# Performance work log

Measured on AMD Instinct MI355X. Metric: run time of the kernel, lower is better.

## Reference

```python
import jax, jax.numpy as jnp
import numpy as np

EPS = 1e-8  # torch cosine_similarity default eps


def setup_inputs() -> dict:
    key = jax.random.key(0)
    k1, k2, k3 = jax.random.split(key, 3)
    bsz, sent_len, cont_dim, mp_dim = 16, 512, 768, 20
    repres = jax.random.normal(k1, (bsz, sent_len, cont_dim), dtype=jnp.float32)
    max_att = jax.random.normal(k2, (bsz, sent_len, cont_dim), dtype=jnp.float32)
    # nn.Parameter initialized uniform_(-1, 1)
    weight = jax.random.uniform(k3, (mp_dim, cont_dim), dtype=jnp.float32, minval=-1.0, maxval=1.0)
    return {"repres": repres, "max_att": max_att, "weight": weight}


def reference(repres, max_att, weight):
    # Original math: a = repres[:,None,:] * w[None], b = max_att[:,None,:] * w[None]
    # cos = <a,b> / (max(||a||,eps) * max(||b||,eps)) along last dim.
    # Fused form: never materialize [N, mp_dim, cont_dim]; contract with w^2 directly.
    bsz, sent_len, cont_dim = repres.shape
    r = repres.reshape(-1, cont_dim)   # [N, D]
    m = max_att.reshape(-1, cont_dim)  # [N, D]
    w2 = weight * weight               # [P, D]
    dot = jnp.einsum('nd,pd->np', r * m, w2)              # [N, P]
    n1 = jnp.sqrt(jnp.einsum('nd,pd->np', r * r, w2))     # [N, P]
    n2 = jnp.sqrt(jnp.einsum('nd,pd->np', m * m, w2))     # [N, P]
    cos = dot / (jnp.maximum(n1, EPS) * jnp.maximum(n2, EPS))
    return cos.reshape(bsz, sent_len, weight.shape[0])
```

## Files before the change

### kernel.cpp

```cpp
#include <hip/hip_runtime.h>
#include <math.h>
#include <stdint.h>

static constexpr int D_DIM   = 768;
static constexpr int NP      = 20;
static constexpr int NROWS   = 8192;
static constexpr int ROWS_PB = 16;
static constexpr int BLOCKS  = NROWS / ROWS_PB;
static constexpr int KW      = 192;
static constexpr int KSLICE  = 32;
static constexpr int NSLICES = KW / KSLICE;

typedef short  short8  __attribute__((ext_vector_type(8)));
typedef float  float4v __attribute__((ext_vector_type(4)));

static constexpr int A_WAVE = 8192;
static constexpr int A_BUF  = 4096;
static constexpr int A_MAT  = 2048;
static constexpr int B_OFF  = 32768;
static constexpr int B_CSTR = 776 * 2;
static constexpr int LDS_SZ = B_OFF + NP * B_CSTR;

__device__ __forceinline__ void async_copy16(const void* g, void* l) {
  __builtin_amdgcn_global_load_lds(
      (const __attribute__((address_space(1))) unsigned int*)(uintptr_t)g,
      (__attribute__((address_space(3))) unsigned int*)(uint32_t)(uintptr_t)l,
      16, 0, 0);
}

__device__ __forceinline__ unsigned short bf16_rne(float x) {
  unsigned u = __float_as_uint(x);
  u += 0x7FFFu + ((u >> 16) & 1u);
  return (unsigned short)(u >> 16);
}
__device__ __forceinline__ float bf16f(unsigned short h) {
  return __uint_as_float(((unsigned)h) << 16);
}

__global__ __launch_bounds__(256) void atte_cos_mfma(
    const float* __restrict__ repres,
    const float* __restrict__ max_att,
    const float* __restrict__ weight,
    float* __restrict__ out)
{
  const int tid  = threadIdx.x;
  const int wave = tid >> 6;
  const int lane = tid & 63;
  const int row0 = blockIdx.x * ROWS_PB;
  const int k0   = wave * KW;
  const int part = lane >> 4;
  const int mrow = lane & 15;

  __shared__ __align__(16) char smem[LDS_SZ];
  char* a_base = smem + wave * A_WAVE;

  auto stage = [&](int s, int b) {
#pragma unroll
    for (int j = 0; j < 2; ++j) {
      const int slot = j * 64 + lane;
      const int row  = slot >> 3;
      const int gp   = slot & 7;
      const int gl   = (gp - 2 * (row & 3)) & 7;
      const float* gr = repres  + (size_t)(row0 + row) * D_DIM + k0 + s * KSLICE + gl * 4;
      const float* gm = max_att + (size_t)(row0 + row) * D_DIM + k0 + s * KSLICE + gl * 4;
      char* la = a_base + b * A_BUF + slot * 16;
      async_copy16(gr, la);
      async_copy16(gm, la + A_MAT);
    }
  };

  stage(0, 0);
  stage(1, 1);

  for (int col = 0; col < NP; ++col) {
#pragma unroll
    for (int j = 0; j < 3; ++j) {
      const int k = j * 256 + tid;
      const float wv = weight[col * D_DIM + k];
      *(unsigned short*)(smem + B_OFF + col * B_CSTR + k * 2) = bf16_rne(wv * wv);
    }
  }

  __syncthreads();

  const int a_off = mrow * 128 + (((part + (mrow & 3)) & 3) * 32);
  const char* b0p = smem + B_OFF + (lane & 15) * B_CSTR + (k0 + part * 8) * 2;
  const int c1col = min(16 + (lane & 15), NP - 1);
  const char* b1p = smem + B_OFF + c1col * B_CSTR + (k0 + part * 8) * 2;

  float4v acc[6] = {};

#pragma unroll
  for (int s = 0; s < NSLICES; ++s) {
    __builtin_amdgcn_s_waitcnt(0x0F74);
    const char* ab = a_base + (s & 1) * A_BUF;

    float rv[8], mv[8];
    *(float4*)&rv[0] = *(const float4*)(ab + a_off);
    *(float4*)&rv[4] = *(const float4*)(ab + a_off + 16);
    *(float4*)&mv[0] = *(const float4*)(ab + A_MAT + a_off);
    *(float4*)&mv[4] = *(const float4*)(ab + A_MAT + a_off + 16);

    short8 a0h, a0l, a1h, a2h;
#pragma unroll
    for (int j = 0; j < 8; ++j) {
      const float pm = rv[j] * mv[j];
      const float pr = rv[j] * rv[j];
      const float pq = mv[j] * mv[j];
      const unsigned short h = bf16_rne(pm);
      a0h[j] = (short)h;
      a0l[j] = (short)bf16_rne(pm - bf16f(h));
      a1h[j] = (short)bf16_rne(pr);
      a2h[j] = (short)bf16_rne(pq);
    }

    const short8 b0 = *(const short8*)(b0p + s * 64);
    const short8 b1 = *(const short8*)(b1p + s * 64);

    acc[0] = __builtin_amdgcn_mfma_f32_16x16x32_bf16(a0h, b0, acc[0], 0, 0, 0);
    acc[0] = __builtin_amdgcn_mfma_f32_16x16x32_bf16(a0l, b0, acc[0], 0, 0, 0);
    acc[1] = __builtin_amdgcn_mfma_f32_16x16x32_bf16(a0h, b1, acc[1], 0, 0, 0);
    acc[1] = __builtin_amdgcn_mfma_f32_16x16x32_bf16(a0l, b1, acc[1], 0, 0, 0);
    acc[2] = __builtin_amdgcn_mfma_f32_16x16x32_bf16(a1h, b0, acc[2], 0, 0, 0);
    acc[3] = __builtin_amdgcn_mfma_f32_16x16x32_bf16(a1h, b1, acc[3], 0, 0, 0);
    acc[4] = __builtin_amdgcn_mfma_f32_16x16x32_bf16(a2h, b0, acc[4], 0, 0, 0);
    acc[5] = __builtin_amdgcn_mfma_f32_16x16x32_bf16(a2h, b1, acc[5], 0, 0, 0);

    if (s + 2 < NSLICES) {
      __builtin_amdgcn_s_waitcnt(0xC07F);
      stage(s + 2, s & 1);
    }
  }

  __syncthreads();
#pragma unroll
  for (int qc = 0; qc < 6; ++qc)
    *(float4v*)(smem + ((qc * 4 + wave) * 64 + lane) * 16) = acc[qc];
  __syncthreads();

  if (wave < 2) {
    const int ct = wave;
    float4v c0 = {}, c1 = {}, c2 = {};
#pragma unroll
    for (int wv = 0; wv < 4; ++wv) {
      c0 += *(const float4v*)(smem + (((0 * 2 + ct) * 4 + wv) * 64 + lane) * 16);
      c1 += *(const float4v*)(smem + (((1 * 2 + ct) * 4 + wv) * 64 + lane) * 16);
      c2 += *(const float4v*)(smem + (((2 * 2 + ct) * 4 + wv) * 64 + lane) * 16);
    }
    const int col = ct * 16 + (lane & 15);
    if (col < NP) {
      const int rbase = row0 + (lane >> 4) * 4;
#pragma unroll
      for (int r = 0; r < 4; ++r) {
        const float n1 = fmaxf(sqrtf(c1[r]), 1e-8f);
        const float n2 = fmaxf(sqrtf(c2[r]), 1e-8f);
        out[(size_t)(rbase + r) * NP + col] = c0[r] / (n1 * n2);
      }
    }
  }
}

extern "C" void kernel_launch(void* const* d_in, const int* in_sizes, int n_in,
                              void* d_out, int out_size, void* d_ws, size_t ws_size,
                              hipStream_t stream) {
  const float* repres  = (const float*)d_in[0];
  const float* max_att = (const float*)d_in[1];
  const float* weight  = (const float*)d_in[2];
  float* out = (float*)d_out;

  atte_cos_mfma<<<BLOCKS, 256, 0, stream>>>(repres, max_att, weight, out);
}
```

Baseline: 88.19 us.

## Replace bf16 MFMA kernel with fp32 FMA kernel staging full rows and squared weights

Replaces the split-bf16 MFMA kernel with an fp32 FMA kernel using 512 threads per block. Each block stages all 16 rows of both inputs in two halves via async global-to-LDS copies, and keeps the full fp32 squared weight table in about 156 KB of dynamic LDS. Each thread accumulates 60 dot products over a k-slice, and partial sums are combined with shuffles and then through LDS scratch. This drops the bf16 hi/lo emulation and the MFMA operand packing, and gains full fp32 accuracy. In exchange, the LDS footprint allows only one block per CU, each block re-reads and re-squares the full weight table, and there is little load/compute overlap.

```diff
diff --git a/kernel.cpp b/kernel.cpp
--- a/kernel.cpp
+++ b/kernel.cpp
@@ -1,25 +1,23 @@
 #include <hip/hip_runtime.h>
 #include <math.h>
 #include <stdint.h>
+
 
 static constexpr int D_DIM   = 768;
 static constexpr int NP      = 20;
 static constexpr int NROWS   = 8192;
 static constexpr int ROWS_PB = 16;
-static constexpr int BLOCKS  = NROWS / ROWS_PB;
-static constexpr int KW      = 192;
-static constexpr int KSLICE  = 32;
-static constexpr int NSLICES = KW / KSLICE;
+static constexpr int NBLK    = NROWS / ROWS_PB;
+static constexpr int NTHR    = 512;
 
-typedef short  short8  __attribute__((ext_vector_type(8)));
-typedef float  float4v __attribute__((ext_vector_type(4)));
+static constexpr int HALF_B  = 1536;
+static constexpr int MAT_B   = ROWS_PB * HALF_B;
+static constexpr int SWEEP_B = 2 * MAT_B;
+static constexpr int W2_OFF  = 2 * SWEEP_B;
+static constexpr int LDS_B   = W2_OFF + NP * D_DIM * 4;
 
-static constexpr int A_WAVE = 8192;
-static constexpr int A_BUF  = 4096;
-static constexpr int A_MAT  = 2048;
-static constexpr int B_OFF  = 32768;
-static constexpr int B_CSTR = 776 * 2;
-static constexpr int LDS_SZ = B_OFF + NP * B_CSTR;
+static constexpr int SCR_K   = 12;
+static constexpr int SCR_RND = 8 * NP * 3 * SCR_K;
 
 __device__ __forceinline__ void async_copy16(const void* g, void* l) {
   __builtin_amdgcn_global_load_lds(
@@ -28,145 +26,142 @@
       16, 0, 0);
 }
 
-__device__ __forceinline__ unsigned short bf16_rne(float x) {
-  unsigned u = __float_as_uint(x);
-  u += 0x7FFFu + ((u >> 16) & 1u);
-  return (unsigned short)(u >> 16);
-}
-__device__ __forceinline__ float bf16f(unsigned short h) {
-  return __uint_as_float(((unsigned)h) << 16);
-}
-
-__global__ __launch_bounds__(256) void atte_cos_mfma(
+__global__ __launch_bounds__(NTHR, 2) void atte_cos_v2(
     const float* __restrict__ repres,
     const float* __restrict__ max_att,
     const float* __restrict__ weight,
     float* __restrict__ out)
 {
+  extern __shared__ __align__(16) char smem[];
   const int tid  = threadIdx.x;
   const int wave = tid >> 6;
   const int lane = tid & 63;
   const int row0 = blockIdx.x * ROWS_PB;
-  const int k0   = wave * KW;
-  const int part = lane >> 4;
-  const int mrow = lane & 15;
 
-  __shared__ __align__(16) char smem[LDS_SZ];
-  char* a_base = smem + wave * A_WAVE;
-
-  auto stage = [&](int s, int b) {
+  auto dma_sweep = [&](int s) {
 #pragma unroll
-    for (int j = 0; j < 2; ++j) {
-      const int slot = j * 64 + lane;
-      const int row  = slot >> 3;
-      const int gp   = slot & 7;
-      const int gl   = (gp - 2 * (row & 3)) & 7;
-      const float* gr = repres  + (size_t)(row0 + row) * D_DIM + k0 + s * KSLICE + gl * 4;
-      const float* gm = max_att + (size_t)(row0 + row) * D_DIM + k0 + s * KSLICE + gl * 4;
-      char* la = a_base + b * A_BUF + slot * 16;
-      async_copy16(gr, la);
-      async_copy16(gm, la + A_MAT);
+    for (int i = 0; i < 6; ++i) {
+      const int ls  = wave * 6144 + i * 1024 + lane * 16;
+      const int mat = ls >= MAT_B;
+      const int off = ls - (mat ? MAT_B : 0);
+      const int r   = off / HALF_B;
+      const int kb  = off - r * HALF_B;
+      const char* src = (const char*)(mat ? max_att : repres)
+                      + (size_t)(row0 + r) * 3072 + (size_t)s * HALF_B + kb;
+      async_copy16(src, smem + s * SWEEP_B + ls);
     }
   };
 
-  stage(0, 0);
-  stage(1, 1);
+  dma_sweep(0);
 
-  for (int col = 0; col < NP; ++col) {
-#pragma unroll
-    for (int j = 0; j < 3; ++j) {
-      const int k = j * 256 + tid;
-      const float wv = weight[col * D_DIM + k];
-      *(unsigned short*)(smem + B_OFF + col * B_CSTR + k * 2) = bf16_rne(wv * wv);
+  {
+    const float4* wsrc = (const float4*)weight;
+    float4* wdst = (float4*)(smem + W2_OFF);
+    for (int idx = tid; idx < NP * D_DIM / 4; idx += NTHR) {
+      float4 w = wsrc[idx];
+      w.x *= w.x; w.y *= w.y; w.z *= w.z; w.w *= w.w;
+      wdst[idx] = w;
     }
   }
 
-  __syncthreads();
+  dma_sweep(1);
 
-  const int a_off = mrow * 128 + (((part + (mrow & 3)) & 3) * 32);
-  const char* b0p = smem + B_OFF + (lane & 15) * B_CSTR + (k0 + part * 8) * 2;
-  const int c1col = min(16 + (lane & 15), NP - 1);
-  const char* b1p = smem + B_OFF + c1col * B_CSTR + (k0 + part * 8) * 2;
+  const int row  = tid >> 5;
+  const int ksub = tid & 31;
 
-  float4v acc[6] = {};
+  float accd[NP], acc1[NP], acc2[NP];
+#pragma unroll
+  for (int p = 0; p < NP; ++p) { accd[p] = 0.f; acc1[p] = 0.f; acc2[p] = 0.f; }
+
+  auto compute_half = [&](const int s) {
+    const char* ar = smem + s * SWEEP_B + row * HALF_B;
+    const char* am = ar + MAT_B;
+    const char* wb = smem + W2_OFF + s * HALF_B;
+#pragma unroll
+    for (int j = 0; j < 3; ++j) {
+      const int g16 = (ksub + 32 * j) * 16;
+      const float4 r4 = *(const float4*)(ar + g16);
+      const float4 m4 = *(const float4*)(am + g16);
+      const float pd0 = r4.x * m4.x, pd1 = r4.y * m4.y, pd2 = r4.z * m4.z, pd3 = r4.w * m4.w;
+      const float p10 = r4.x * r4.x, p11 = r4.y * r4.y, p12 = r4.z * r4.z, p13 = r4.w * r4.w;
+      const float p20 = m4.x * m4.x, p21 = m4.y * m4.y, p22 = m4.z * m4.z, p23 = m4.w * m4.w;
+#pragma unroll
+      for (int p = 0; p < NP; ++p) {
+        const float4 w4 = *(const float4*)(wb + p * 3072 + g16);
+        accd[p] = fmaf(pd3, w4.w, fmaf(pd2, w4.z, fmaf(pd1, w4.y, fmaf(pd0, w4.x, accd[p]))));
+        acc1[p] = fmaf(p13, w4.w, fmaf(p12, w4.z, fmaf(p11, w4.y, fmaf(p10, w4.x, acc1[p]))));
+        acc2[p] = fmaf(p23, w4.w, fmaf(p22, w4.z, fmaf(p21, w4.y, fmaf(p20, w4.x, acc2[p]))));
+      }
+    }
+  };
+
+  __builtin_amdgcn_sched_barrier(0);
+  __builtin_amdgcn_s_waitcnt(0x0076);
+  __builtin_amdgcn_s_barrier();
+  __builtin_amdgcn_sched_barrier(0);
+  compute_half(0);
+
+  __builtin_amdgcn_sched_barrier(0);
+  __builtin_amdgcn_s_waitcnt(0x0F70);
+  __builtin_amdgcn_s_barrier();
+  __builtin_amdgcn_sched_barrier(0);
+  compute_half(1);
 
 #pragma unroll
-  for (int s = 0; s < NSLICES; ++s) {
-    __builtin_amdgcn_s_waitcnt(0x0F74);
-    const char* ab = a_base + (s & 1) * A_BUF;
+  for (int p = 0; p < NP; ++p) {
+    accd[p] += __shfl_xor(accd[p], 16); acc1[p] += __shfl_xor(acc1[p], 16); acc2[p] += __shfl_xor(acc2[p], 16);
+    accd[p] += __shfl_xor(accd[p],  8); acc1[p] += __shfl_xor(acc1[p],  8); acc2[p] += __shfl_xor(acc2[p],  8);
+  }
 
-    float rv[8], mv[8];
-    *(float4*)&rv[0] = *(const float4*)(ab + a_off);
-    *(float4*)&rv[4] = *(const float4*)(ab + a_off + 16);
-    *(float4*)&mv[0] = *(const float4*)(ab + A_MAT + a_off);
-    *(float4*)&mv[4] = *(const float4*)(ab + A_MAT + a_off + 16);
+  __builtin_amdgcn_sched_barrier(0);
+  __builtin_amdgcn_s_waitcnt(0xC07F);
+  __builtin_amdgcn_s_barrier();
+  __builtin_amdgcn_sched_barrier(0);
 
-    short8 a0h, a0l, a1h, a2h;
+  float* scr = (float*)smem;
+  if (ksub < 8) {
+    const int rnd = row >> 3, lrow = row & 7;
+    float* base = scr + rnd * SCR_RND + (lrow * NP * 3) * SCR_K + ksub;
 #pragma unroll
-    for (int j = 0; j < 8; ++j) {
-      const float pm = rv[j] * mv[j];
-      const float pr = rv[j] * rv[j];
-      const float pq = mv[j] * mv[j];
-      const unsigned short h = bf16_rne(pm);
-      a0h[j] = (short)h;
-      a0l[j] = (short)bf16_rne(pm - bf16f(h));
-      a1h[j] = (short)bf16_rne(pr);
-      a2h[j] = (short)bf16_rne(pq);
-    }
-
-    const short8 b0 = *(const short8*)(b0p + s * 64);
-    const short8 b1 = *(const short8*)(b1p + s * 64);
-
-    acc[0] = __builtin_amdgcn_mfma_f32_16x16x32_bf16(a0h, b0, acc[0], 0, 0, 0);
-    acc[0] = __builtin_amdgcn_mfma_f32_16x16x32_bf16(a0l, b0, acc[0], 0, 0, 0);
-    acc[1] = __builtin_amdgcn_mfma_f32_16x16x32_bf16(a0h, b1, acc[1], 0, 0, 0);
-    acc[1] = __builtin_amdgcn_mfma_f32_16x16x32_bf16(a0l, b1, acc[1], 0, 0, 0);
-    acc[2] = __builtin_amdgcn_mfma_f32_16x16x32_bf16(a1h, b0, acc[2], 0, 0, 0);
-    acc[3] = __builtin_amdgcn_mfma_f32_16x16x32_bf16(a1h, b1, acc[3], 0, 0, 0);
-    acc[4] = __builtin_amdgcn_mfma_f32_16x16x32_bf16(a2h, b0, acc[4], 0, 0, 0);
-    acc[5] = __builtin_amdgcn_mfma_f32_16x16x32_bf16(a2h, b1, acc[5], 0, 0, 0);
-
-    if (s + 2 < NSLICES) {
-      __builtin_amdgcn_s_waitcnt(0xC07F);
-      stage(s + 2, s & 1);
+    for (int p = 0; p < NP; ++p) {
+      base[(p * 3 + 0) * SCR_K] = accd[p];
+      base[(p * 3 + 1) * SCR_K] = acc1[p];
+      base[(p * 3 + 2) * SCR_K] = acc2[p];
     }
   }
 
-  __syncthreads();
+  __builtin_amdgcn_sched_barrier(0);
+  __builtin_amdgcn_s_waitcnt(0xC07F);
+  __builtin_amdgcn_s_barrier();
+  __builtin_amdgcn_sched_barrier(0);
+
+  if (tid < 2 * 8 * NP) {
+    const int rnd = tid / 160;
+    const int t   = tid - rnd * 160;
+    const int rr  = t / NP;
+    const int p   = t - rr * NP;
+    const float* b = scr + rnd * SCR_RND + ((rr * NP + p) * 3) * SCR_K;
+    float s0 = 0.f, s1 = 0.f, s2 = 0.f;
 #pragma unroll
-  for (int qc = 0; qc < 6; ++qc)
-    *(float4v*)(smem + ((qc * 4 + wave) * 64 + lane) * 16) = acc[qc];
-  __syncthreads();
-
-  if (wave < 2) {
-    const int ct = wave;
-    float4v c0 = {}, c1 = {}, c2 = {};
-#pragma unroll
-    for (int wv = 0; wv < 4; ++wv) {
-      c0 += *(const float4v*)(smem + (((0 * 2 + ct) * 4 + wv) * 64 + lane) * 16);
-      c1 += *(const float4v*)(smem + (((1 * 2 + ct) * 4 + wv) * 64 + lane) * 16);
-      c2 += *(const float4v*)(smem + (((2 * 2 + ct) * 4 + wv) * 64 + lane) * 16);
+    for (int c = 0; c < 8; ++c) {
+      s0 += b[0 * SCR_K + c]; s1 += b[1 * SCR_K + c]; s2 += b[2 * SCR_K + c];
     }
-    const int col = ct * 16 + (lane & 15);
-    if (col < NP) {
-      const int rbase = row0 + (lane >> 4) * 4;
-#pragma unroll
-      for (int r = 0; r < 4; ++r) {
-        const float n1 = fmaxf(sqrtf(c1[r]), 1e-8f);
-        const float n2 = fmaxf(sqrtf(c2[r]), 1e-8f);
-        out[(size_t)(rbase + r) * NP + col] = c0[r] / (n1 * n2);
-      }
-    }
+    const float n1 = fmaxf(sqrtf(s1), 1e-8f);
+    const float n2 = fmaxf(sqrtf(s2), 1e-8f);
+    out[(size_t)(row0 + rnd * 8 + rr) * NP + p] = s0 / (n1 * n2);
   }
 }
 
 extern "C" void kernel_launch(void* const* d_in, const int* in_sizes, int n_in,
                               void* d_out, int out_size, void* d_ws, size_t ws_size,
                               hipStream_t stream) {
-  const float* repres  = (const float*)d_in[0];
-  const float* max_att = (const float*)d_in[1];
-  const float* weight  = (const float*)d_in[2];
-  float* out = (float*)d_out;
-
-  atte_cos_mfma<<<BLOCKS, 256, 0, stream>>>(repres, max_att, weight, out);
+  static bool attr_set = false;
+  if (!attr_set) {
+    hipFuncSetAttribute(reinterpret_cast<const void*>(atte_cos_v2),
+                        hipFuncAttributeMaxDynamicSharedMemorySize, LDS_B);
+    attr_set = true;
+  }
+  atte_cos_v2<<<NBLK, NTHR, LDS_B, stream>>>(
+      (const float*)d_in[0], (const float*)d_in[1],
+      (const float*)d_in[2], (float*)d_out);
 }
```

New measurement: 102.9 us. 16.7% more time.
